# Performance work log

Measured on AMD Instinct MI355X. Metric: run time of the kernel, lower is better.

The kernel has to match this reference:

```python
import jax, jax.numpy as jnp
import numpy as np

D_K = 128
NEG_MAX = float(np.finfo(np.float32).max)  # original uses -finfo(float32).max


def setup_inputs() -> dict:
    key = jax.random.key(0)
    kq, kk, kv, km = jax.random.split(key, 4)
    B, S, D = 16, 2048, D_K
    q = jax.random.normal(kq, (B, S, D), dtype=jnp.float32)
    k = jax.random.normal(kk, (B, S, D), dtype=jnp.float32)
    v = jax.random.normal(kv, (B, S, D), dtype=jnp.float32)
    mask = jax.random.randint(km, (B, S, S), 0, 2).astype(jnp.bool_)
    return {"q": q, "k": k, "v": v, "mask": mask}


def reference(q, k, v, mask):
    # scores: [B, S, S] = q @ k^T / sqrt(d_k)
    scale = 1.0 / np.sqrt(D_K).astype(np.float32)
    scores = jnp.einsum('bqd,bkd->bqk', q, k) * scale
    scores = jnp.where(mask, -NEG_MAX, scores)  # masked_fill with -float32 max
    attn = jax.nn.softmax(scores, axis=2)
    return jnp.einsum('bqk,bkd->bqd', attn, v)
```

## Files before the change

kernel.cpp:

```cpp
#include <hip/hip_runtime.h>

#define NTHREADS 256

typedef __attribute__((ext_vector_type(8))) short bf16x8;
typedef __attribute__((ext_vector_type(4))) short bf16x4;
typedef __attribute__((ext_vector_type(4))) float f32x4;
typedef __attribute__((ext_vector_type(2))) unsigned uint2v;
typedef __attribute__((ext_vector_type(4))) unsigned uint4v;

constexpr int kB = 16, kS = 2048, kD = 128;
constexpr int QBLK = 128, KBLK = 32;
constexpr int MSTRIDE = 36;
constexpr float kNegMax = -3.402823466e38f;
constexpr float kMClamp = -1e30f;
constexpr float kDeferThr = 8.0f;

__device__ __forceinline__ unsigned cvt_pk(float lo, float hi) {
    unsigned r;
    asm("v_cvt_pk_bf16_f32 %0, %1, %2" : "=v"(r) : "v"(lo), "v"(hi));
    return r;
}

__device__ __forceinline__ f32x4 mfma16(bf16x4 a, bf16x4 b, f32x4 c) {
#if __has_builtin(__builtin_amdgcn_mfma_f32_16x16x16bf16_1k)
    return __builtin_amdgcn_mfma_f32_16x16x16bf16_1k(a, b, c, 0, 0, 0);
#else
    asm("v_mfma_f32_16x16x16_bf16 %0, %1, %2, %0" : "+v"(c) : "v"(a), "v"(b));
    return c;
#endif
}

#define SWZ(bytecol, row) ((bytecol) ^ (((row) & 7) << 4))
#define KEYV(d) ((((d) & 7) ^ (((d) >> 2) & 7)) & 7)

template<int SPLIT>
__global__ __launch_bounds__(NTHREADS, 2)
void attn_fwd(const float* __restrict__ q, const float* __restrict__ k,
              const float* __restrict__ v, const int* __restrict__ mask,
              float* __restrict__ out, float* __restrict__ ws)
{
    __shared__ __align__(16) char smem[20992];
    char* K_lds  = smem;
    char* VT_lds = smem + 8192;
    unsigned char* M_lds = (unsigned char*)(smem + 16384);

    const int tid = threadIdx.x, lane = tid & 63, w = tid >> 6;
    const int l15 = lane & 15, lg = lane >> 4;

    const int bid = (int)blockIdx.x;
    int b, qbase, kbase;
    if (SPLIT == 1) {
        int swz = (bid & 7) * 32 + (bid >> 3);
        b = swz >> 4; qbase = (swz & 15) * QBLK; kbase = 0;
    } else {
        int swz = (bid & 7) * 64 + (bid >> 3);
        b = swz >> 5;
        int rem = swz & 31;
        qbase = (rem >> 1) * QBLK;
        kbase = (rem & 1) * (kS / 2);
    }
    const int nrounds = (SPLIT == 1) ? (kS / KBLK) : (kS / KBLK / 2);

    const float scale = 0.08838834764831845f * 1.4426950408889634f;
    bf16x8 qf[2][4];
    #pragma unroll
    for (int qs = 0; qs < 2; ++qs) {
        const float* qp = q + ((size_t)(b*kS + qbase + w*32 + qs*16 + l15)) * kD;
        #pragma unroll
        for (int kk = 0; kk < 4; ++kk) {
            float4 a = *(const float4*)(qp + kk*32 + lg*8);
            float4 c = *(const float4*)(qp + kk*32 + lg*8 + 4);
            uint4v pk = { cvt_pk(a.x*scale, a.y*scale), cvt_pk(a.z*scale, a.w*scale),
                          cvt_pk(c.x*scale, c.y*scale), cvt_pk(c.z*scale, c.w*scale) };
            qf[qs][kk] = __builtin_bit_cast(bf16x8, pk);
        }
    }

    f32x4 acc[2][8];
    #pragma unroll
    for (int qs = 0; qs < 2; ++qs)
        #pragma unroll
        for (int d = 0; d < 8; ++d) acc[qs][d] = f32x4{0.f,0.f,0.f,0.f};
    float m_r[2] = {kMClamp, kMClamp};
    float l_r[2] = {0.f, 0.f};

    const float* kbat = k + (size_t)b * kS * kD;
    const float* vbat = v + (size_t)b * kS * kD;
    const int*   mbat = mask + ((size_t)b * kS + qbase) * kS;

    const int kg = tid >> 5, dg = tid & 31;

    float4 kreg[2][2];
    float4 vreg[4];
    int4   mreg[4];

    auto LOAD = [&](int kt0) {
        #pragma unroll
        for (int c = 0; c < 2; ++c) {
            int chunk = c * 256 + tid;
            int row = chunk >> 4, col8 = chunk & 15;
            const float4* ptr = (const float4*)(kbat + (size_t)(kt0 + row)*kD + col8*8);
            kreg[c][0] = ptr[0];
            kreg[c][1] = ptr[1];
        }
        #pragma unroll
        for (int r = 0; r < 4; ++r)
            vreg[r] = *(const float4*)(vbat + (size_t)(kt0 + kg*4 + r)*kD + dg*4);
        #pragma unroll
        for (int c = 0; c < 4; ++c) {
            int idx = c * 256 + tid;
            int mrow = idx >> 3, mc4 = idx & 7;
            mreg[c] = *(const int4*)(mbat + (size_t)mrow*kS + kt0 + mc4*4);
        }
    };

    auto STORE = [&]() {
        #pragma unroll
        for (int c = 0; c < 2; ++c) {
            int chunk = c * 256 + tid;
            int row = chunk >> 4, col8 = chunk & 15;
            uint4v pk = { cvt_pk(kreg[c][0].x, kreg[c][0].y), cvt_pk(kreg[c][0].z, kreg[c][0].w),
                          cvt_pk(kreg[c][1].x, kreg[c][1].y), cvt_pk(kreg[c][1].z, kreg[c][1].w) };
            *(uint4v*)(K_lds + row*256 + SWZ(col8*16, row)) = pk;
        }
        #pragma unroll
        for (int jj = 0; jj < 4; ++jj) {
            int d = dg * 4 + jj;
            int col = (d >> 6) * 64 + kg * 8;
            uint2v pk = { cvt_pk((&vreg[0].x)[jj], (&vreg[1].x)[jj]),
                          cvt_pk((&vreg[2].x)[jj], (&vreg[3].x)[jj]) };
            *(uint2v*)(VT_lds + (d & 63)*128 + (col ^ (KEYV(d) << 4))) = pk;
        }
        #pragma unroll
        for (int c = 0; c < 4; ++c) {
            int idx = c * 256 + tid;
            int mrow = idx >> 3, mc4 = idx & 7;
            unsigned pk = (unsigned)(mreg[c].x != 0)
                        | ((unsigned)(mreg[c].y != 0) << 8)
                        | ((unsigned)(mreg[c].z != 0) << 16)
                        | ((unsigned)(mreg[c].w != 0) << 24);
            *(unsigned*)(M_lds + mrow*MSTRIDE + mc4*4) = pk;
        }
    };

    LOAD(kbase);

    for (int t = 0; t < nrounds; ++t) {
        __syncthreads();
        STORE();
        __syncthreads();
        if (t + 1 < nrounds) LOAD(kbase + (t + 1) * KBLK);

        f32x4 z[2][2];
        #pragma unroll
        for (int qs = 0; qs < 2; ++qs)
            #pragma unroll
            for (int kt = 0; kt < 2; ++kt) z[qs][kt] = f32x4{0.f,0.f,0.f,0.f};
        #pragma unroll
        for (int kt = 0; kt < 2; ++kt) {
            bf16x8 kf[4];
            int krow = kt*16 + l15;
            #pragma unroll
            for (int kk = 0; kk < 4; ++kk)
                kf[kk] = *(const bf16x8*)(K_lds + krow*256 + SWZ(kk*64 + lg*16, krow));
            #pragma unroll
            for (int qs = 0; qs < 2; ++qs)
                #pragma unroll
                for (int kk = 0; kk < 4; ++kk)
                    z[qs][kt] = __builtin_amdgcn_mfma_f32_16x16x32_bf16(kf[kk], qf[qs][kk], z[qs][kt], 0, 0, 0);
        }

        bf16x4 pfA[2], pfB[2];
        #pragma unroll
        for (int qs = 0; qs < 2; ++qs) {
            const int mrowb = (w*32 + qs*16 + l15) * MSTRIDE;
            float mx = kNegMax;
            #pragma unroll
            for (int kt = 0; kt < 2; ++kt) {
                unsigned nib = *(const unsigned*)(M_lds + mrowb + kt*16 + lg*4);
                #pragma unroll
                for (int i = 0; i < 4; ++i) {
                    float sv = ((nib >> (8*i)) & 0xFFu) ? kNegMax : z[qs][kt][i];
                    z[qs][kt][i] = sv;
                    mx = fmaxf(mx, sv);
                }
            }
            mx = fmaxf(mx, __shfl_xor(mx, 16));
            mx = fmaxf(mx, __shfl_xor(mx, 32));
            if (!__all(mx <= m_r[qs] + kDeferThr)) {
                float mnew = fmaxf(m_r[qs], mx);
                float corr = exp2f(m_r[qs] - mnew);
                l_r[qs] *= corr;
                #pragma unroll
                for (int d = 0; d < 8; ++d) acc[qs][d] *= corr;
                m_r[qs] = mnew;
            }
            float p00 = exp2f(z[qs][0][0] - m_r[qs]);
            float p01 = exp2f(z[qs][0][1] - m_r[qs]);
            float p02 = exp2f(z[qs][0][2] - m_r[qs]);
            float p03 = exp2f(z[qs][0][3] - m_r[qs]);
            float p10 = exp2f(z[qs][1][0] - m_r[qs]);
            float p11 = exp2f(z[qs][1][1] - m_r[qs]);
            float p12 = exp2f(z[qs][1][2] - m_r[qs]);
            float p13 = exp2f(z[qs][1][3] - m_r[qs]);
            float rs = ((p00 + p01) + (p02 + p03)) + ((p10 + p11) + (p12 + p13));
            rs += __shfl_xor(rs, 16);
            rs += __shfl_xor(rs, 32);
            l_r[qs] += rs;
            uint2v pa = { cvt_pk(p00, p01), cvt_pk(p02, p03) };
            uint2v pb = { cvt_pk(p10, p11), cvt_pk(p12, p13) };
            pfA[qs] = __builtin_bit_cast(bf16x4, pa);
            pfB[qs] = __builtin_bit_cast(bf16x4, pb);
        }

        #pragma unroll
        for (int dblk = 0; dblk < 8; ++dblk) {
            int d = dblk*16 + l15;
            int rowb = (d & 63) * 128;
            int half = (d >> 6) * 64;
            int key = KEYV(d) << 4;
            bf16x4 vf0 = *(const bf16x4*)(VT_lds + rowb + ((half + lg*8) ^ key));
            bf16x4 vf1 = *(const bf16x4*)(VT_lds + rowb + ((half + 32 + lg*8) ^ key));
            #pragma unroll
            for (int qs = 0; qs < 2; ++qs) {
                acc[qs][dblk] = mfma16(vf0, pfA[qs], acc[qs][dblk]);
                acc[qs][dblk] = mfma16(vf1, pfB[qs], acc[qs][dblk]);
            }
        }
    }

    if (SPLIT == 1) {
        #pragma unroll
        for (int qs = 0; qs < 2; ++qs) {
            float inv = 1.0f / l_r[qs];
            float* op = out + ((size_t)(b*kS + qbase + w*32 + qs*16 + l15)) * kD;
            #pragma unroll
            for (int dblk = 0; dblk < 8; ++dblk) {
                float4 r;
                r.x = acc[qs][dblk][0] * inv;
                r.y = acc[qs][dblk][1] * inv;
                r.z = acc[qs][dblk][2] * inv;
                r.w = acc[qs][dblk][3] * inv;
                *(float4*)(op + dblk*16 + lg*4) = r;
            }
        }
    } else {
        const int half = (kbase != 0);
        #pragma unroll
        for (int qs = 0; qs < 2; ++qs) {
            const size_t row = (size_t)half * (kB*kS) + (size_t)b*kS + qbase + w*32 + qs*16 + l15;
            float* op = ws + row * kD;
            #pragma unroll
            for (int dblk = 0; dblk < 8; ++dblk) {
                float4 r;
                r.x = acc[qs][dblk][0]; r.y = acc[qs][dblk][1];
                r.z = acc[qs][dblk][2]; r.w = acc[qs][dblk][3];
                *(float4*)(op + dblk*16 + lg*4) = r;
            }
            if (lg == 0) {
                float* ml = ws + (size_t)2*kB*kS*kD;
                ml[row*2 + 0] = m_r[qs];
                ml[row*2 + 1] = l_r[qs];
            }
        }
    }
}

__global__ __launch_bounds__(NTHREADS)
void attn_merge(const float* __restrict__ ws, float* __restrict__ out)
{
    const float* ml = ws + (size_t)2*kB*kS*kD;
    const int tid = threadIdx.x;
    const size_t r = (size_t)blockIdx.x * 8 + (tid >> 5);
    const int c = (tid & 31) * 4;
    float m0 = ml[r*2 + 0],               l0 = ml[r*2 + 1];
    float m1 = ml[((size_t)kB*kS + r)*2], l1 = ml[((size_t)kB*kS + r)*2 + 1];
    float mS = fmaxf(m0, m1);
    float e0 = exp2f(m0 - mS), e1 = exp2f(m1 - mS);
    float inv = 1.0f / (l0*e0 + l1*e1);
    float4 o0 = *(const float4*)(ws + r*kD + c);
    float4 o1 = *(const float4*)(ws + (size_t)kB*kS*kD + r*kD + c);
    float4 rr;
    rr.x = (o0.x*e0 + o1.x*e1) * inv;
    rr.y = (o0.y*e0 + o1.y*e1) * inv;
    rr.z = (o0.z*e0 + o1.z*e1) * inv;
    rr.w = (o0.w*e0 + o1.w*e1) * inv;
    *(float4*)(out + r*kD + c) = rr;
}

extern "C" void kernel_launch(void* const* d_in, const int* in_sizes, int n_in,
                              void* d_out, int out_size, void* d_ws, size_t ws_size,
                              hipStream_t stream) {
    const float* q = (const float*)d_in[0];
    const float* k = (const float*)d_in[1];
    const float* v = (const float*)d_in[2];
    const int* mask = (const int*)d_in[3];
    float* out = (float*)d_out;
    const size_t wsNeeded = (size_t)2*kB*kS*kD*4 + (size_t)2*kB*kS*2*4;
    if (ws_size >= wsNeeded) {
        attn_fwd<2><<<dim3(kB * (kS/QBLK) * 2), dim3(NTHREADS), 0, stream>>>(
            q, k, v, mask, out, (float*)d_ws);
        attn_merge<<<dim3(kB*kS/8), dim3(NTHREADS), 0, stream>>>((const float*)d_ws, out);
    } else {
        attn_fwd<1><<<dim3(kB * (kS/QBLK)), dim3(NTHREADS), 0, stream>>>(
            q, k, v, mask, out, nullptr);
    }
}
```

Measured before the change: 107.2 us.

## Double-buffer LDS tiles and add MFMA priority hints in attention loop

Keeps two LDS buffers for the K, V-transpose and mask tiles. Each round now stores the next tile into the alternate buffer after its own compute, so the per-round barrier count drops from two to one and the global-load latency overlaps more compute. It also raises wave priority around the MFMA sections with s_setprio. The cost is doubled LDS use (about 42KB per block), which could limit occupancy at two blocks per CU, and the unrolled loop assumes an even round count.

```diff
diff --git a/kernel.cpp b/kernel.cpp
--- a/kernel.cpp
+++ b/kernel.cpp
@@ -11,6 +11,7 @@
 constexpr int kB = 16, kS = 2048, kD = 128;
 constexpr int QBLK = 128, KBLK = 32;
 constexpr int MSTRIDE = 36;
+constexpr int BUFSZ = 20992;
 constexpr float kNegMax = -3.402823466e38f;
 constexpr float kMClamp = -1e30f;
 constexpr float kDeferThr = 8.0f;
@@ -39,10 +40,7 @@
               const float* __restrict__ v, const int* __restrict__ mask,
               float* __restrict__ out, float* __restrict__ ws)
 {
-    __shared__ __align__(16) char smem[20992];
-    char* K_lds  = smem;
-    char* VT_lds = smem + 8192;
-    unsigned char* M_lds = (unsigned char*)(smem + 16384);
+    __shared__ __align__(16) char smem[2 * BUFSZ];
 
     const int tid = threadIdx.x, lane = tid & 63, w = tid >> 6;
     const int l15 = lane & 15, lg = lane >> 4;
@@ -114,14 +112,14 @@
         }
     };
 
-    auto STORE = [&]() {
+    auto STORE = [&](char* Kd, char* VTd, unsigned char* Md) {
         #pragma unroll
         for (int c = 0; c < 2; ++c) {
             int chunk = c * 256 + tid;
             int row = chunk >> 4, col8 = chunk & 15;
             uint4v pk = { cvt_pk(kreg[c][0].x, kreg[c][0].y), cvt_pk(kreg[c][0].z, kreg[c][0].w),
                           cvt_pk(kreg[c][1].x, kreg[c][1].y), cvt_pk(kreg[c][1].z, kreg[c][1].w) };
-            *(uint4v*)(K_lds + row*256 + SWZ(col8*16, row)) = pk;
+            *(uint4v*)(Kd + row*256 + SWZ(col8*16, row)) = pk;
         }
         #pragma unroll
         for (int jj = 0; jj < 4; ++jj) {
@@ -129,7 +127,7 @@
             int col = (d >> 6) * 64 + kg * 8;
             uint2v pk = { cvt_pk((&vreg[0].x)[jj], (&vreg[1].x)[jj]),
                           cvt_pk((&vreg[2].x)[jj], (&vreg[3].x)[jj]) };
-            *(uint2v*)(VT_lds + (d & 63)*128 + (col ^ (KEYV(d) << 4))) = pk;
+            *(uint2v*)(VTd + (d & 63)*128 + (col ^ (KEYV(d) << 4))) = pk;
         }
         #pragma unroll
         for (int c = 0; c < 4; ++c) {
@@ -139,36 +137,35 @@
                         | ((unsigned)(mreg[c].y != 0) << 8)
                         | ((unsigned)(mreg[c].z != 0) << 16)
                         | ((unsigned)(mreg[c].w != 0) << 24);
-            *(unsigned*)(M_lds + mrow*MSTRIDE + mc4*4) = pk;
+            *(unsigned*)(Md + mrow*MSTRIDE + mc4*4) = pk;
         }
     };
 
-    LOAD(kbase);
-
-    for (int t = 0; t < nrounds; ++t) {
-        __syncthreads();
-        STORE();
-        __syncthreads();
-        if (t + 1 < nrounds) LOAD(kbase + (t + 1) * KBLK);
+    auto ROUND = [&](char* Kb, char* VTb, unsigned char* Mb,
+                     char* Kn, char* VTn, unsigned char* Mn, int t) {
+        const bool has_next = (t + 1 < nrounds);
+        if (has_next) LOAD(kbase + (t + 1) * KBLK);
 
         f32x4 z[2][2];
         #pragma unroll
         for (int qs = 0; qs < 2; ++qs)
             #pragma unroll
             for (int kt = 0; kt < 2; ++kt) z[qs][kt] = f32x4{0.f,0.f,0.f,0.f};
+        __builtin_amdgcn_s_setprio(1);
         #pragma unroll
         for (int kt = 0; kt < 2; ++kt) {
             bf16x8 kf[4];
             int krow = kt*16 + l15;
             #pragma unroll
             for (int kk = 0; kk < 4; ++kk)
-                kf[kk] = *(const bf16x8*)(K_lds + krow*256 + SWZ(kk*64 + lg*16, krow));
+                kf[kk] = *(const bf16x8*)(Kb + krow*256 + SWZ(kk*64 + lg*16, krow));
             #pragma unroll
             for (int qs = 0; qs < 2; ++qs)
                 #pragma unroll
                 for (int kk = 0; kk < 4; ++kk)
                     z[qs][kt] = __builtin_amdgcn_mfma_f32_16x16x32_bf16(kf[kk], qf[qs][kk], z[qs][kt], 0, 0, 0);
         }
+        __builtin_amdgcn_s_setprio(0);
 
         bf16x4 pfA[2], pfB[2];
         #pragma unroll
@@ -177,7 +174,7 @@
             float mx = kNegMax;
             #pragma unroll
             for (int kt = 0; kt < 2; ++kt) {
-                unsigned nib = *(const unsigned*)(M_lds + mrowb + kt*16 + lg*4);
+                unsigned nib = *(const unsigned*)(Mb + mrowb + kt*16 + lg*4);
                 #pragma unroll
                 for (int i = 0; i < 4; ++i) {
                     float sv = ((nib >> (8*i)) & 0xFFu) ? kNegMax : z[qs][kt][i];
@@ -213,20 +210,39 @@
             pfB[qs] = __builtin_bit_cast(bf16x4, pb);
         }
 
+        __builtin_amdgcn_s_setprio(1);
         #pragma unroll
         for (int dblk = 0; dblk < 8; ++dblk) {
             int d = dblk*16 + l15;
             int rowb = (d & 63) * 128;
             int half = (d >> 6) * 64;
             int key = KEYV(d) << 4;
-            bf16x4 vf0 = *(const bf16x4*)(VT_lds + rowb + ((half + lg*8) ^ key));
-            bf16x4 vf1 = *(const bf16x4*)(VT_lds + rowb + ((half + 32 + lg*8) ^ key));
+            bf16x4 vf0 = *(const bf16x4*)(VTb + rowb + ((half + lg*8) ^ key));
+            bf16x4 vf1 = *(const bf16x4*)(VTb + rowb + ((half + 32 + lg*8) ^ key));
             #pragma unroll
             for (int qs = 0; qs < 2; ++qs) {
                 acc[qs][dblk] = mfma16(vf0, pfA[qs], acc[qs][dblk]);
                 acc[qs][dblk] = mfma16(vf1, pfB[qs], acc[qs][dblk]);
             }
         }
+        __builtin_amdgcn_s_setprio(0);
+
+        if (has_next) STORE(Kn, VTn, Mn);
+        __syncthreads();
+    };
+
+    char* K0 = smem,          * VT0 = smem + 8192;
+    unsigned char* M0 = (unsigned char*)(smem + 16384);
+    char* K1 = smem + BUFSZ,  * VT1 = smem + BUFSZ + 8192;
+    unsigned char* M1 = (unsigned char*)(smem + BUFSZ + 16384);
+
+    LOAD(kbase);
+    STORE(K0, VT0, M0);
+    __syncthreads();
+
+    for (int t = 0; t < nrounds; t += 2) {
+        ROUND(K0, VT0, M0, K1, VT1, M1, t);
+        ROUND(K1, VT1, M1, K0, VT0, M0, t + 1);
     }
 
     if (SPLIT == 1) {
```

Measured after the change: 108.6 us. No clear change (+1.3%).
